# Kernel tuning notes

Measured on AMD Instinct MI355X. Metric: run time of the kernel, lower is better.

## Reference

```python
import jax, jax.numpy as jnp
import numpy as np

B, T, D, H = 2, 2048, 1024, 16
DK = D // H  # 64
LN_EPS = 1e-5


def softmax_one(x, axis=-1):
    # softmax with an extra +1 in the denominator (allows 'attend to nothing')
    x = x - jax.lax.stop_gradient(jnp.max(x, axis=axis, keepdims=True))
    ex = jnp.exp(x)
    return ex / (1.0 + jnp.sum(ex, axis=axis, keepdims=True))


def setup_inputs() -> dict:
    rng = jax.random.key(0)
    ks = jax.random.split(rng, 16)
    s = 0.02  # param init scale
    return {
        "query": jax.random.normal(ks[0], (B, T, D), jnp.float32),
        "key": jax.random.normal(ks[1], (B, T, D), jnp.float32),
        "value": jax.random.normal(ks[2], (B, T, D), jnp.float32),
        "Wq": jax.random.normal(ks[3], (D, D), jnp.float32) * s,
        "bq": jnp.zeros((D,), jnp.float32),
        "Wk": jax.random.normal(ks[4], (D, D), jnp.float32) * s,
        "bk": jnp.zeros((D,), jnp.float32),
        "Wv": jax.random.normal(ks[5], (D, D), jnp.float32) * s,
        "bv": jnp.zeros((D,), jnp.float32),
        "Wo": jax.random.normal(ks[6], (D, D), jnp.float32) * s,
        "bo": jnp.zeros((D,), jnp.float32),
        "gamma": jnp.ones((D,), jnp.float32),
        "beta": jnp.zeros((D,), jnp.float32),
    }


def reference(query, key, value, Wq, bq, Wk, bk, Wv, bv, Wo, bo, gamma, beta):
    # qkv projections; torch Linear: y = x @ W.T + b
    q = (query @ Wq.T + bq).reshape(B, T, H, DK).transpose(0, 2, 1, 3)  # b h t d
    k = (key @ Wk.T + bk).reshape(B, T, H, DK).transpose(0, 2, 1, 3)
    v = (value @ Wv.T + bv).reshape(B, T, H, DK).transpose(0, 2, 1, 3)

    scores = jnp.einsum("bhqd,bhkd->bhqk", q, k) / np.sqrt(DK).astype(np.float32)
    attn = softmax_one(scores, axis=-1)  # mask=None path; dropout = identity (eval)

    x = jnp.einsum("bhqk,bhkd->bhqd", attn, v)  # [B,H,T,DK]
    x = x.transpose(0, 2, 1, 3).reshape(B, T, D)
    out = x @ Wo.T + bo

    # residual + LayerNorm
    y = query + out
    mu = jnp.mean(y, axis=-1, keepdims=True)
    var = jnp.mean(jnp.square(y - mu), axis=-1, keepdims=True)
    y = (y - mu) * jax.lax.rsqrt(var + LN_EPS) * gamma + beta
    return (y, attn)
```

## Files before the change

### kernel.cpp

```cpp
#include <hip/hip_runtime.h>
#include <hip/hip_bf16.h>
#include <math.h>

#define Bb 2
#define Tt 2048
#define Dd 1024
#define Hh 16
#define DKk 64

typedef __bf16 bf16_t;
typedef __bf16 bf16x8 __attribute__((ext_vector_type(8)));
typedef __bf16 bf16x4 __attribute__((ext_vector_type(4)));
typedef float f32x4 __attribute__((ext_vector_type(4)));

__device__ __forceinline__ void async16(const void* gsrc, void* ldst) {
  void* g = const_cast<void*>(gsrc);
  __builtin_amdgcn_global_load_lds(
      (__attribute__((address_space(1))) void*)g,
      (__attribute__((address_space(3))) void*)ldst, 16, 0, 0);
}

__device__ __forceinline__ bf16x8 cvt8(const float4 a, const float4 b) {
  bf16x8 o;
  o[0] = (bf16_t)a.x; o[1] = (bf16_t)a.y; o[2] = (bf16_t)a.z; o[3] = (bf16_t)a.w;
  o[4] = (bf16_t)b.x; o[5] = (bf16_t)b.y; o[6] = (bf16_t)b.z; o[7] = (bf16_t)b.w;
  return o;
}

#define LDSW(p, row, ch) \
  (*(const bf16x8*)((const char*)(p) + (row) * 128 + ((((ch) ^ (row)) & 7) << 4)))

#define BM 128
#define BN 128
#define BK 64

__global__ __launch_bounds__(256) void gemm_f32_bt_bias(
    const float* __restrict__ A, const float* __restrict__ Bw,
    const float* __restrict__ bias, bf16_t* __restrict__ C,
    int M, int N, int K) {
  __shared__ bf16_t As[BM * BK];
  __shared__ bf16_t Bs[BN * BK];
  const int tid = threadIdx.x;
  const int lane = tid & 63;
  const int w = tid >> 6;
  const int wy = w >> 1, wx = w & 1;
  const int m0 = blockIdx.y * BM, n0 = blockIdx.x * BN;
  const int q = lane >> 4, cc = lane & 15;
  const int srow = lane >> 3;
  const int scol = (lane & 7) * 8;

  f32x4 acc[4][4] = {};

  for (int k0 = 0; k0 < K; k0 += BK) {
    __syncthreads();
#pragma unroll
    for (int i = 0; i < 4; ++i) {
      const int row = (w * 4 + i) * 8 + srow;
      const float* ap = A + (size_t)(m0 + row) * K + k0 + scol;
      const float* bp = Bw + (size_t)(n0 + row) * K + k0 + scol;
      *(bf16x8*)(As + row * BK + scol) =
          cvt8(*(const float4*)ap, *(const float4*)(ap + 4));
      *(bf16x8*)(Bs + row * BK + scol) =
          cvt8(*(const float4*)bp, *(const float4*)(bp + 4));
    }
    __syncthreads();
#pragma unroll
    for (int kk = 0; kk < 2; ++kk) {
      bf16x8 af[4], bfr[4];
#pragma unroll
      for (int i = 0; i < 4; ++i)
        af[i] = *(const bf16x8*)(As + (wy * 64 + i * 16 + cc) * BK + kk * 32 + q * 8);
#pragma unroll
      for (int j = 0; j < 4; ++j)
        bfr[j] = *(const bf16x8*)(Bs + (wx * 64 + j * 16 + cc) * BK + kk * 32 + q * 8);
#pragma unroll
      for (int i = 0; i < 4; ++i)
#pragma unroll
        for (int j = 0; j < 4; ++j)
          acc[i][j] = __builtin_amdgcn_mfma_f32_16x16x32_bf16(af[i], bfr[j], acc[i][j], 0, 0, 0);
    }
  }

#pragma unroll
  for (int j = 0; j < 4; ++j) {
    const int col = n0 + wx * 64 + j * 16 + cc;
    const float bv = bias[col];
#pragma unroll
    for (int i = 0; i < 4; ++i) {
      const int row = m0 + wy * 64 + i * 16 + q * 4;
#pragma unroll
      for (int r = 0; r < 4; ++r)
        C[(size_t)(row + r) * N + col] = (bf16_t)(acc[i][j][r] + bv);
    }
  }
}

__global__ __launch_bounds__(256) void gemm_f32_bt_bias_vt(
    const float* __restrict__ A, const float* __restrict__ Bw,
    const float* __restrict__ bias, bf16_t* __restrict__ C,
    int M, int N, int K) {
  __shared__ bf16_t As[BM * BK];
  __shared__ bf16_t Bs[BN * BK];
  const int tid = threadIdx.x;
  const int lane = tid & 63;
  const int w = tid >> 6;
  const int wy = w >> 1, wx = w & 1;
  const int m0 = blockIdx.y * BM, n0 = blockIdx.x * BN;
  const int q = lane >> 4, cc = lane & 15;
  const int srow = lane >> 3;
  const int scol = (lane & 7) * 8;

  f32x4 acc[4][4] = {};

  for (int k0 = 0; k0 < K; k0 += BK) {
    __syncthreads();
#pragma unroll
    for (int i = 0; i < 4; ++i) {
      const int row = (w * 4 + i) * 8 + srow;
      const float* ap = A + (size_t)(m0 + row) * K + k0 + scol;
      const float* bp = Bw + (size_t)(n0 + row) * K + k0 + scol;
      *(bf16x8*)(As + row * BK + scol) =
          cvt8(*(const float4*)ap, *(const float4*)(ap + 4));
      *(bf16x8*)(Bs + row * BK + scol) =
          cvt8(*(const float4*)bp, *(const float4*)(bp + 4));
    }
    __syncthreads();
#pragma unroll
    for (int kk = 0; kk < 2; ++kk) {
      bf16x8 af[4], bfr[4];
#pragma unroll
      for (int i = 0; i < 4; ++i)
        af[i] = *(const bf16x8*)(As + (wy * 64 + i * 16 + cc) * BK + kk * 32 + q * 8);
#pragma unroll
      for (int j = 0; j < 4; ++j)
        bfr[j] = *(const bf16x8*)(Bs + (wx * 64 + j * 16 + cc) * BK + kk * 32 + q * 8);
#pragma unroll
      for (int i = 0; i < 4; ++i)
#pragma unroll
        for (int j = 0; j < 4; ++j)
          acc[i][j] = __builtin_amdgcn_mfma_f32_16x16x32_bf16(af[i], bfr[j], acc[i][j], 0, 0, 0);
    }
  }

  const int bdx = m0 >> 11;
  const int t00 = (m0 & (Tt - 1)) + wy * 64;
#pragma unroll
  for (int j = 0; j < 4; ++j) {
    const int col = n0 + wx * 64 + j * 16 + cc;
    const float bv = bias[col];
    const size_t rowbase = ((size_t)(bdx * Dd + col)) * Tt;
#pragma unroll
    for (int i = 0; i < 4; ++i) {
      const int t0 = t00 + i * 16 + q * 4;
      bf16x4 pk;
#pragma unroll
      for (int r = 0; r < 4; ++r) pk[r] = (bf16_t)(acc[i][j][r] + bv);
      *(bf16x4*)(C + rowbase + t0) = pk;
    }
  }
}

__global__ __launch_bounds__(256) void gemm_bf16a_f32b_bias(
    const bf16_t* __restrict__ A, const float* __restrict__ Bw,
    const float* __restrict__ bias, bf16_t* __restrict__ C,
    int M, int N, int K) {
  __shared__ bf16_t As[BM * BK];
  __shared__ bf16_t Bs[BN * BK];
  const int tid = threadIdx.x;
  const int lane = tid & 63;
  const int w = tid >> 6;
  const int wy = w >> 1, wx = w & 1;
  const int m0 = blockIdx.y * BM, n0 = blockIdx.x * BN;
  const int q = lane >> 4, cc = lane & 15;
  const int srow = lane >> 3;
  const int scol = (lane & 7) * 8;

  f32x4 acc[4][4] = {};

  for (int k0 = 0; k0 < K; k0 += BK) {
    __syncthreads();
#pragma unroll
    for (int i = 0; i < 4; ++i) {
      const int r0 = w * 32 + i * 8;
      async16(A + (size_t)(m0 + r0 + srow) * K + k0 + scol, As + r0 * BK);
    }
#pragma unroll
    for (int i = 0; i < 4; ++i) {
      const int row = (w * 4 + i) * 8 + srow;
      const float* bp = Bw + (size_t)(n0 + row) * K + k0 + scol;
      *(bf16x8*)(Bs + row * BK + scol) =
          cvt8(*(const float4*)bp, *(const float4*)(bp + 4));
    }
    __syncthreads();
#pragma unroll
    for (int kk = 0; kk < 2; ++kk) {
      bf16x8 af[4], bfr[4];
#pragma unroll
      for (int i = 0; i < 4; ++i)
        af[i] = *(const bf16x8*)(As + (wy * 64 + i * 16 + cc) * BK + kk * 32 + q * 8);
#pragma unroll
      for (int j = 0; j < 4; ++j)
        bfr[j] = *(const bf16x8*)(Bs + (wx * 64 + j * 16 + cc) * BK + kk * 32 + q * 8);
#pragma unroll
      for (int i = 0; i < 4; ++i)
#pragma unroll
        for (int j = 0; j < 4; ++j)
          acc[i][j] = __builtin_amdgcn_mfma_f32_16x16x32_bf16(af[i], bfr[j], acc[i][j], 0, 0, 0);
    }
  }

#pragma unroll
  for (int j = 0; j < 4; ++j) {
    const int col = n0 + wx * 64 + j * 16 + cc;
    const float bv = bias[col];
#pragma unroll
    for (int i = 0; i < 4; ++i) {
      const int row = m0 + wy * 64 + i * 16 + q * 4;
#pragma unroll
      for (int r = 0; r < 4; ++r)
        C[(size_t)(row + r) * N + col] = (bf16_t)(acc[i][j][r] + bv);
    }
  }
}

__global__ __launch_bounds__(256) void attn_fused(
    const bf16_t* __restrict__ Qm, const bf16_t* __restrict__ Km,
    const bf16_t* __restrict__ Vt_g,
    float* __restrict__ attn_out,
    bf16_t* __restrict__ Xb) {
  __shared__ bf16_t Qs[64 * 64];
  __shared__ bf16_t Ks[2][64 * 64];
  __shared__ bf16_t Vs[2][64 * 64];
  __shared__ bf16_t Ps[64 * 64];

  const int tid = threadIdx.x;
  const int lane = tid & 63;
  const int w = tid >> 6;
  const int qt = blockIdx.x, h = blockIdx.y, b = blockIdx.z;
  const int q = lane >> 4, cc = lane & 15;
  const size_t base = (size_t)b * Tt * Dd + (size_t)h * DKk;
  const size_t vbase = ((size_t)(b * Hh + h) * DKk) * Tt;
  const int srow = lane >> 3;
  const int gcol = ((lane & 7) ^ srow) * 8;
  const float CL = 0.18033688f;
  const float C2 = 11.54156028f;

#pragma unroll
  for (int i = 0; i < 2; ++i) {
    const int r0 = w * 16 + i * 8;
    async16(Qm + base + (size_t)(qt * 64 + r0 + srow) * Dd + gcol, Qs + r0 * 64);
    async16(Km + base + (size_t)(r0 + srow) * Dd + gcol, Ks[0] + r0 * 64);
  }

  float Mp[4], Lp[4];
#pragma unroll
  for (int r = 0; r < 4; ++r) { Mp[r] = -3.0e38f; Lp[r] = 0.f; }

  for (int kt = 0; kt < 32; ++kt) {
    __syncthreads();
    if (kt < 31) {
      bf16_t* kd = Ks[(kt + 1) & 1];
#pragma unroll
      for (int i = 0; i < 2; ++i) {
        const int r0 = w * 16 + i * 8;
        async16(Km + base + (size_t)((kt + 1) * 64 + r0 + srow) * Dd + gcol, kd + r0 * 64);
      }
    }
    const bf16_t* kc = Ks[kt & 1];
    f32x4 acc[4] = {};
    __builtin_amdgcn_s_setprio(1);
#pragma unroll
    for (int kk = 0; kk < 2; ++kk) {
      const bf16x8 af = LDSW(Qs, w * 16 + cc, kk * 4 + q);
#pragma unroll
      for (int j = 0; j < 4; ++j) {
        const bf16x8 bfr = LDSW(kc, j * 16 + cc, kk * 4 + q);
        acc[j] = __builtin_amdgcn_mfma_f32_16x16x32_bf16(af, bfr, acc[j], 0, 0, 0);
      }
    }
    __builtin_amdgcn_s_setprio(0);
#pragma unroll
    for (int r = 0; r < 4; ++r) {
      Mp[r] = fmaxf(Mp[r], fmaxf(fmaxf(acc[0][r], acc[1][r]),
                                 fmaxf(acc[2][r], acc[3][r])));
      Lp[r] += exp2f(fmaf(acc[0][r], CL, -C2)) + exp2f(fmaf(acc[1][r], CL, -C2)) +
               exp2f(fmaf(acc[2][r], CL, -C2)) + exp2f(fmaf(acc[3][r], CL, -C2));
    }
  }

  float inv1[4];
#pragma unroll
  for (int r = 0; r < 4; ++r) {
    float mx = Mp[r];
#pragma unroll
    for (int msk = 1; msk < 16; msk <<= 1) mx = fmaxf(mx, __shfl_xor(mx, msk));
    float ls = Lp[r];
#pragma unroll
    for (int msk = 1; msk < 16; msk <<= 1) ls += __shfl_xor(ls, msk);
    inv1[r] = 1.0f / (exp2f(fmaf(mx, CL, -C2)) + ls);
  }

#pragma unroll
  for (int i = 0; i < 2; ++i) {
    const int r0 = w * 16 + i * 8;
    async16(Km + base + (size_t)(r0 + srow) * Dd + gcol, Ks[0] + r0 * 64);
    async16(Vt_g + vbase + (size_t)(r0 + srow) * Tt + gcol, Vs[0] + r0 * 64);
  }

  f32x4 xacc[4] = {};
  const size_t arowbase = ((size_t)(b * Hh + h) * Tt + (size_t)qt * 64) * Tt;

  for (int kt = 0; kt < 32; ++kt) {
    __syncthreads();
    if (kt < 31) {
      bf16_t* kd = Ks[(kt + 1) & 1];
      bf16_t* vd = Vs[(kt + 1) & 1];
#pragma unroll
      for (int i = 0; i < 2; ++i) {
        const int r0 = w * 16 + i * 8;
        async16(Km + base + (size_t)((kt + 1) * 64 + r0 + srow) * Dd + gcol, kd + r0 * 64);
        async16(Vt_g + vbase + (size_t)(r0 + srow) * Tt + (kt + 1) * 64 + gcol, vd + r0 * 64);
      }
    }
    const bf16_t* kc = Ks[kt & 1];
    const bf16_t* vc = Vs[kt & 1];

    f32x4 acc[4] = {};
    __builtin_amdgcn_s_setprio(1);
#pragma unroll
    for (int kk = 0; kk < 2; ++kk) {
      const bf16x8 af = LDSW(Qs, w * 16 + cc, kk * 4 + q);
#pragma unroll
      for (int j = 0; j < 4; ++j) {
        const bf16x8 bfr = LDSW(kc, j * 16 + cc, kk * 4 + q);
        acc[j] = __builtin_amdgcn_mfma_f32_16x16x32_bf16(af, bfr, acc[j], 0, 0, 0);
      }
    }
    __builtin_amdgcn_s_setprio(0);

#pragma unroll
    for (int j = 0; j < 4; ++j) {
      const int pcol = j * 16 + cc;
#pragma unroll
      for (int r = 0; r < 4; ++r) {
        const int prow = w * 16 + q * 4 + r;
        const float p = exp2f(fmaf(acc[j][r], CL, -C2)) * inv1[r];
        attn_out[arowbase + (size_t)prow * Tt + kt * 64 + pcol] = p;
        *(bf16_t*)((char*)Ps + prow * 128 + ((pcol * 2) ^ ((prow & 7) << 4))) = (bf16_t)p;
      }
    }

    __builtin_amdgcn_s_setprio(1);
#pragma unroll
    for (int kk = 0; kk < 2; ++kk) {
      const bf16x8 af = LDSW(Ps, w * 16 + cc, kk * 4 + q);
#pragma unroll
      for (int j = 0; j < 4; ++j) {
        const bf16x8 bfr = LDSW(vc, j * 16 + cc, kk * 4 + q);
        xacc[j] = __builtin_amdgcn_mfma_f32_16x16x32_bf16(af, bfr, xacc[j], 0, 0, 0);
      }
    }
    __builtin_amdgcn_s_setprio(0);
  }

#pragma unroll
  for (int j = 0; j < 4; ++j)
#pragma unroll
    for (int r = 0; r < 4; ++r) {
      const int row = qt * 64 + w * 16 + q * 4 + r;
      Xb[base + (size_t)row * Dd + j * 16 + cc] = (bf16_t)xacc[j][r];
    }
}

__global__ __launch_bounds__(256) void ln_kernel(
    const float* __restrict__ resid, const bf16_t* __restrict__ O,
    const float* __restrict__ gamma, const float* __restrict__ beta,
    float* __restrict__ out) {
  const int row = blockIdx.x;
  const int tid = threadIdx.x;
  const size_t roff = (size_t)row * Dd + tid * 4;
  const float4 rv = *(const float4*)(resid + roff);
  const bf16x4 ov = *(const bf16x4*)(O + roff);
  const float y0 = rv.x + (float)ov.x;
  const float y1 = rv.y + (float)ov.y;
  const float y2 = rv.z + (float)ov.z;
  const float y3 = rv.w + (float)ov.w;
  float s = y0 + y1 + y2 + y3;
  float s2 = y0 * y0 + y1 * y1 + y2 * y2 + y3 * y3;
#pragma unroll
  for (int msk = 1; msk < 64; msk <<= 1) {
    s += __shfl_xor(s, msk);
    s2 += __shfl_xor(s2, msk);
  }
  __shared__ float red[8];
  const int w = tid >> 6;
  if ((tid & 63) == 0) { red[w] = s; red[4 + w] = s2; }
  __syncthreads();
  s = red[0] + red[1] + red[2] + red[3];
  s2 = red[4] + red[5] + red[6] + red[7];
  const float mu = s * (1.f / Dd);
  const float rstd = rsqrtf(s2 * (1.f / Dd) - mu * mu + 1e-5f);
  const float4 gv = *(const float4*)(gamma + tid * 4);
  const float4 bv = *(const float4*)(beta + tid * 4);
  float4 o;
  o.x = (y0 - mu) * rstd * gv.x + bv.x;
  o.y = (y1 - mu) * rstd * gv.y + bv.y;
  o.z = (y2 - mu) * rstd * gv.z + bv.z;
  o.w = (y3 - mu) * rstd * gv.w + bv.w;
  *(float4*)(out + roff) = o;
}

extern "C" void kernel_launch(void* const* d_in, const int* in_sizes, int n_in,
                              void* d_out, int out_size, void* d_ws, size_t ws_size,
                              hipStream_t stream) {
  const float* query = (const float*)d_in[0];
  const float* key = (const float*)d_in[1];
  const float* value = (const float*)d_in[2];
  const float* Wq = (const float*)d_in[3];
  const float* bq = (const float*)d_in[4];
  const float* Wk = (const float*)d_in[5];
  const float* bk = (const float*)d_in[6];
  const float* Wv = (const float*)d_in[7];
  const float* bv = (const float*)d_in[8];
  const float* Wo = (const float*)d_in[9];
  const float* bo = (const float*)d_in[10];
  const float* gamma = (const float*)d_in[11];
  const float* beta = (const float*)d_in[12];

  float* y_out = (float*)d_out;
  float* attn_out = y_out + (size_t)Bb * Tt * Dd;

  char* p = (char*)d_ws;
  const size_t nTD = (size_t)Bb * Tt * Dd;
  bf16_t* Qb = (bf16_t*)p;  p += nTD * 2;
  bf16_t* Kb = (bf16_t*)p;  p += nTD * 2;
  bf16_t* VtG = (bf16_t*)p; p += nTD * 2;
  bf16_t* Xb = (bf16_t*)p;  p += nTD * 2;
  bf16_t* Ob = (bf16_t*)p;  p += nTD * 2;

  dim3 gg(Dd / BN, (Bb * Tt) / BM);
  gemm_f32_bt_bias<<<gg, 256, 0, stream>>>(query, Wq, bq, Qb, Bb * Tt, Dd, Dd);
  gemm_f32_bt_bias<<<gg, 256, 0, stream>>>(key, Wk, bk, Kb, Bb * Tt, Dd, Dd);
  gemm_f32_bt_bias_vt<<<gg, 256, 0, stream>>>(value, Wv, bv, VtG, Bb * Tt, Dd, Dd);

  dim3 ga(Tt / 64, Hh, Bb);
  attn_fused<<<ga, 256, 0, stream>>>(Qb, Kb, VtG, attn_out, Xb);

  gemm_bf16a_f32b_bias<<<gg, 256, 0, stream>>>(Xb, Wo, bo, Ob, Bb * Tt, Dd, Dd);

  ln_kernel<<<Bb * Tt, 256, 0, stream>>>(query, Ob, gamma, beta, y_out);
}
```

Measured before the change: 921.9 us.

## Merge QKV GEMMs into one launch, shrink tiles, stage attn probs in LDS

The three projection GEMMs become a single launch over a z-dimension, and both GEMM kernels shrink the M tile from 128 to 64 so more blocks run per launch. In attention, the fp32 probabilities are staged in each wave's slice of the just-consumed K buffer, then written to the attn output as coalesced 16-byte stores instead of scattered scalar stores. The bf16 A operand for the PV MFMA is read back from that same staging, which removes the separate P buffer. The cost is an extra barrier per key tile and more LDS round-trips, and the smaller GEMM tiles give less data reuse per block.

```diff
diff --git a/kernel.cpp b/kernel.cpp
--- a/kernel.cpp
+++ b/kernel.cpp
@@ -30,195 +30,164 @@
 #define LDSW(p, row, ch) \
   (*(const bf16x8*)((const char*)(p) + (row) * 128 + ((((ch) ^ (row)) & 7) << 4)))
 
-#define BM 128
-#define BN 128
-#define BK 64
-
-__global__ __launch_bounds__(256) void gemm_f32_bt_bias(
-    const float* __restrict__ A, const float* __restrict__ Bw,
-    const float* __restrict__ bias, bf16_t* __restrict__ C,
-    int M, int N, int K) {
-  __shared__ bf16_t As[BM * BK];
-  __shared__ bf16_t Bs[BN * BK];
+#define GM 4096
+#define GN 1024
+#define GK 1024
+#define BM2 64
+#define BN2 128
+#define BK2 64
+
+__global__ __launch_bounds__(256) void gemm_qkv(
+    const float* __restrict__ Aq, const float* __restrict__ Ak,
+    const float* __restrict__ Av, const float* __restrict__ Wqp,
+    const float* __restrict__ Wkp, const float* __restrict__ Wvp,
+    const float* __restrict__ bqp, const float* __restrict__ bkp,
+    const float* __restrict__ bvp, bf16_t* __restrict__ Cq,
+    bf16_t* __restrict__ Ck, bf16_t* __restrict__ Cv) {
+  __shared__ bf16_t As[BM2 * BK2];
+  __shared__ bf16_t Bs[BN2 * BK2];
+  const int z = blockIdx.z;
+  const float* A = (z == 0) ? Aq : (z == 1) ? Ak : Av;
+  const float* Bw = (z == 0) ? Wqp : (z == 1) ? Wkp : Wvp;
+  const float* bias = (z == 0) ? bqp : (z == 1) ? bkp : bvp;
+
   const int tid = threadIdx.x;
   const int lane = tid & 63;
   const int w = tid >> 6;
   const int wy = w >> 1, wx = w & 1;
-  const int m0 = blockIdx.y * BM, n0 = blockIdx.x * BN;
+  const int m0 = blockIdx.y * BM2, n0 = blockIdx.x * BN2;
   const int q = lane >> 4, cc = lane & 15;
   const int srow = lane >> 3;
   const int scol = (lane & 7) * 8;
 
-  f32x4 acc[4][4] = {};
-
-  for (int k0 = 0; k0 < K; k0 += BK) {
-    __syncthreads();
+  f32x4 acc[2][4] = {};
+
+  for (int k0 = 0; k0 < GK; k0 += BK2) {
+    __syncthreads();
+#pragma unroll
+    for (int i = 0; i < 2; ++i) {
+      const int row = w * 16 + i * 8 + srow;
+      const float* ap = A + (size_t)(m0 + row) * GK + k0 + scol;
+      *(bf16x8*)(As + row * BK2 + scol) =
+          cvt8(*(const float4*)ap, *(const float4*)(ap + 4));
+    }
 #pragma unroll
     for (int i = 0; i < 4; ++i) {
       const int row = (w * 4 + i) * 8 + srow;
-      const float* ap = A + (size_t)(m0 + row) * K + k0 + scol;
-      const float* bp = Bw + (size_t)(n0 + row) * K + k0 + scol;
-      *(bf16x8*)(As + row * BK + scol) =
-          cvt8(*(const float4*)ap, *(const float4*)(ap + 4));
-      *(bf16x8*)(Bs + row * BK + scol) =
+      const float* bp = Bw + (size_t)(n0 + row) * GK + k0 + scol;
+      *(bf16x8*)(Bs + row * BK2 + scol) =
           cvt8(*(const float4*)bp, *(const float4*)(bp + 4));
     }
     __syncthreads();
 #pragma unroll
     for (int kk = 0; kk < 2; ++kk) {
-      bf16x8 af[4], bfr[4];
-#pragma unroll
-      for (int i = 0; i < 4; ++i)
-        af[i] = *(const bf16x8*)(As + (wy * 64 + i * 16 + cc) * BK + kk * 32 + q * 8);
+      bf16x8 af[2], bfr[4];
+#pragma unroll
+      for (int i = 0; i < 2; ++i)
+        af[i] = *(const bf16x8*)(As + (wy * 32 + i * 16 + cc) * BK2 + kk * 32 + q * 8);
 #pragma unroll
       for (int j = 0; j < 4; ++j)
-        bfr[j] = *(const bf16x8*)(Bs + (wx * 64 + j * 16 + cc) * BK + kk * 32 + q * 8);
-#pragma unroll
-      for (int i = 0; i < 4; ++i)
+        bfr[j] = *(const bf16x8*)(Bs + (wx * 64 + j * 16 + cc) * BK2 + kk * 32 + q * 8);
+#pragma unroll
+      for (int i = 0; i < 2; ++i)
 #pragma unroll
         for (int j = 0; j < 4; ++j)
           acc[i][j] = __builtin_amdgcn_mfma_f32_16x16x32_bf16(af[i], bfr[j], acc[i][j], 0, 0, 0);
     }
   }
 
-#pragma unroll
-  for (int j = 0; j < 4; ++j) {
-    const int col = n0 + wx * 64 + j * 16 + cc;
-    const float bv = bias[col];
-#pragma unroll
-    for (int i = 0; i < 4; ++i) {
-      const int row = m0 + wy * 64 + i * 16 + q * 4;
-#pragma unroll
-      for (int r = 0; r < 4; ++r)
-        C[(size_t)(row + r) * N + col] = (bf16_t)(acc[i][j][r] + bv);
-    }
-  }
-}
-
-__global__ __launch_bounds__(256) void gemm_f32_bt_bias_vt(
-    const float* __restrict__ A, const float* __restrict__ Bw,
-    const float* __restrict__ bias, bf16_t* __restrict__ C,
-    int M, int N, int K) {
-  __shared__ bf16_t As[BM * BK];
-  __shared__ bf16_t Bs[BN * BK];
+  if (z < 2) {
+    bf16_t* C = z ? Ck : Cq;
+#pragma unroll
+    for (int j = 0; j < 4; ++j) {
+      const int col = n0 + wx * 64 + j * 16 + cc;
+      const float bv = bias[col];
+#pragma unroll
+      for (int i = 0; i < 2; ++i) {
+        const int row = m0 + wy * 32 + i * 16 + q * 4;
+#pragma unroll
+        for (int r = 0; r < 4; ++r)
+          C[(size_t)(row + r) * GN + col] = (bf16_t)(acc[i][j][r] + bv);
+      }
+    }
+  } else {
+    const int bdx = m0 >> 11;
+    const int t00 = (m0 & (Tt - 1)) + wy * 32;
+#pragma unroll
+    for (int j = 0; j < 4; ++j) {
+      const int col = n0 + wx * 64 + j * 16 + cc;
+      const float bv = bias[col];
+      const size_t rowbase = ((size_t)(bdx * Dd + col)) * Tt;
+#pragma unroll
+      for (int i = 0; i < 2; ++i) {
+        const int t0 = t00 + i * 16 + q * 4;
+        bf16x4 pk;
+#pragma unroll
+        for (int r = 0; r < 4; ++r) pk[r] = (bf16_t)(acc[i][j][r] + bv);
+        *(bf16x4*)(Cv + rowbase + t0) = pk;
+      }
+    }
+  }
+}
+
+__global__ __launch_bounds__(256) void gemm_obf16(
+    const bf16_t* __restrict__ A, const float* __restrict__ Bw,
+    const float* __restrict__ bias, bf16_t* __restrict__ C) {
+  __shared__ bf16_t As[BM2 * BK2];
+  __shared__ bf16_t Bs[BN2 * BK2];
   const int tid = threadIdx.x;
   const int lane = tid & 63;
   const int w = tid >> 6;
   const int wy = w >> 1, wx = w & 1;
-  const int m0 = blockIdx.y * BM, n0 = blockIdx.x * BN;
+  const int m0 = blockIdx.y * BM2, n0 = blockIdx.x * BN2;
   const int q = lane >> 4, cc = lane & 15;
   const int srow = lane >> 3;
   const int scol = (lane & 7) * 8;
 
-  f32x4 acc[4][4] = {};
-
-  for (int k0 = 0; k0 < K; k0 += BK) {
-    __syncthreads();
+  f32x4 acc[2][4] = {};
+
+  for (int k0 = 0; k0 < GK; k0 += BK2) {
+    __syncthreads();
+#pragma unroll
+    for (int i = 0; i < 2; ++i) {
+      const int r0 = w * 16 + i * 8;
+      async16(A + (size_t)(m0 + r0 + srow) * GK + k0 + scol, As + r0 * BK2);
+    }
 #pragma unroll
     for (int i = 0; i < 4; ++i) {
       const int row = (w * 4 + i) * 8 + srow;
-      const float* ap = A + (size_t)(m0 + row) * K + k0 + scol;
-      const float* bp = Bw + (size_t)(n0 + row) * K + k0 + scol;
-      *(bf16x8*)(As + row * BK + scol) =
-          cvt8(*(const float4*)ap, *(const float4*)(ap + 4));
-      *(bf16x8*)(Bs + row * BK + scol) =
+      const float* bp = Bw + (size_t)(n0 + row) * GK + k0 + scol;
+      *(bf16x8*)(Bs + row * BK2 + scol) =
           cvt8(*(const float4*)bp, *(const float4*)(bp + 4));
     }
     __syncthreads();
 #pragma unroll
     for (int kk = 0; kk < 2; ++kk) {
-      bf16x8 af[4], bfr[4];
-#pragma unroll
-      for (int i = 0; i < 4; ++i)
-        af[i] = *(const bf16x8*)(As + (wy * 64 + i * 16 + cc) * BK + kk * 32 + q * 8);
+      bf16x8 af[2], bfr[4];
+#pragma unroll
+      for (int i = 0; i < 2; ++i)
+        af[i] = *(const bf16x8*)(As + (wy * 32 + i * 16 + cc) * BK2 + kk * 32 + q * 8);
 #pragma unroll
       for (int j = 0; j < 4; ++j)
-        bfr[j] = *(const bf16x8*)(Bs + (wx * 64 + j * 16 + cc) * BK + kk * 32 + q * 8);
-#pragma unroll
-      for (int i = 0; i < 4; ++i)
+        bfr[j] = *(const bf16x8*)(Bs + (wx * 64 + j * 16 + cc) * BK2 + kk * 32 + q * 8);
+#pragma unroll
+      for (int i = 0; i < 2; ++i)
 #pragma unroll
         for (int j = 0; j < 4; ++j)
           acc[i][j] = __builtin_amdgcn_mfma_f32_16x16x32_bf16(af[i], bfr[j], acc[i][j], 0, 0, 0);
     }
   }
 
-  const int bdx = m0 >> 11;
-  const int t00 = (m0 & (Tt - 1)) + wy * 64;
 #pragma unroll
   for (int j = 0; j < 4; ++j) {
     const int col = n0 + wx * 64 + j * 16 + cc;
     const float bv = bias[col];
-    const size_t rowbase = ((size_t)(bdx * Dd + col)) * Tt;
-#pragma unroll
-    for (int i = 0; i < 4; ++i) {
-      const int t0 = t00 + i * 16 + q * 4;
-      bf16x4 pk;
-#pragma unroll
-      for (int r = 0; r < 4; ++r) pk[r] = (bf16_t)(acc[i][j][r] + bv);
-      *(bf16x4*)(C + rowbase + t0) = pk;
-    }
-  }
-}
-
-__global__ __launch_bounds__(256) void gemm_bf16a_f32b_bias(
-    const bf16_t* __restrict__ A, const float* __restrict__ Bw,
-    const float* __restrict__ bias, bf16_t* __restrict__ C,
-    int M, int N, int K) {
-  __shared__ bf16_t As[BM * BK];
-  __shared__ bf16_t Bs[BN * BK];
-  const int tid = threadIdx.x;
-  const int lane = tid & 63;
-  const int w = tid >> 6;
-  const int wy = w >> 1, wx = w & 1;
-  const int m0 = blockIdx.y * BM, n0 = blockIdx.x * BN;
-  const int q = lane >> 4, cc = lane & 15;
-  const int srow = lane >> 3;
-  const int scol = (lane & 7) * 8;
-
-  f32x4 acc[4][4] = {};
-
-  for (int k0 = 0; k0 < K; k0 += BK) {
-    __syncthreads();
-#pragma unroll
-    for (int i = 0; i < 4; ++i) {
-      const int r0 = w * 32 + i * 8;
-      async16(A + (size_t)(m0 + r0 + srow) * K + k0 + scol, As + r0 * BK);
-    }
-#pragma unroll
-    for (int i = 0; i < 4; ++i) {
-      const int row = (w * 4 + i) * 8 + srow;
-      const float* bp = Bw + (size_t)(n0 + row) * K + k0 + scol;
-      *(bf16x8*)(Bs + row * BK + scol) =
-          cvt8(*(const float4*)bp, *(const float4*)(bp + 4));
-    }
-    __syncthreads();
-#pragma unroll
-    for (int kk = 0; kk < 2; ++kk) {
-      bf16x8 af[4], bfr[4];
-#pragma unroll
-      for (int i = 0; i < 4; ++i)
-        af[i] = *(const bf16x8*)(As + (wy * 64 + i * 16 + cc) * BK + kk * 32 + q * 8);
-#pragma unroll
-      for (int j = 0; j < 4; ++j)
-        bfr[j] = *(const bf16x8*)(Bs + (wx * 64 + j * 16 + cc) * BK + kk * 32 + q * 8);
-#pragma unroll
-      for (int i = 0; i < 4; ++i)
-#pragma unroll
-        for (int j = 0; j < 4; ++j)
-          acc[i][j] = __builtin_amdgcn_mfma_f32_16x16x32_bf16(af[i], bfr[j], acc[i][j], 0, 0, 0);
-    }
-  }
-
-#pragma unroll
-  for (int j = 0; j < 4; ++j) {
-    const int col = n0 + wx * 64 + j * 16 + cc;
-    const float bv = bias[col];
-#pragma unroll
-    for (int i = 0; i < 4; ++i) {
-      const int row = m0 + wy * 64 + i * 16 + q * 4;
+#pragma unroll
+    for (int i = 0; i < 2; ++i) {
+      const int row = m0 + wy * 32 + i * 16 + q * 4;
 #pragma unroll
       for (int r = 0; r < 4; ++r)
-        C[(size_t)(row + r) * N + col] = (bf16_t)(acc[i][j][r] + bv);
+        C[(size_t)(row + r) * GN + col] = (bf16_t)(acc[i][j][r] + bv);
     }
   }
 }
@@ -231,7 +200,6 @@
   __shared__ bf16_t Qs[64 * 64];
   __shared__ bf16_t Ks[2][64 * 64];
   __shared__ bf16_t Vs[2][64 * 64];
-  __shared__ bf16_t Ps[64 * 64];
 
   const int tid = threadIdx.x;
   const int lane = tid & 63;
@@ -242,6 +210,8 @@
   const size_t vbase = ((size_t)(b * Hh + h) * DKk) * Tt;
   const int srow = lane >> 3;
   const int gcol = ((lane & 7) ^ srow) * 8;
+  const int l2 = lane >> 2;
+  const int lc = lane & 3;
   const float CL = 0.18033688f;
   const float C2 = 11.54156028f;
 
@@ -338,29 +308,48 @@
     }
     __builtin_amdgcn_s_setprio(0);
 
-#pragma unroll
-    for (int j = 0; j < 4; ++j) {
-      const int pcol = j * 16 + cc;
-#pragma unroll
-      for (int r = 0; r < 4; ++r) {
-        const int prow = w * 16 + q * 4 + r;
-        const float p = exp2f(fmaf(acc[j][r], CL, -C2)) * inv1[r];
-        attn_out[arowbase + (size_t)prow * Tt + kt * 64 + pcol] = p;
-        *(bf16_t*)((char*)Ps + prow * 128 + ((pcol * 2) ^ ((prow & 7) << 4))) = (bf16_t)p;
-      }
-    }
-
-    __builtin_amdgcn_s_setprio(1);
-#pragma unroll
-    for (int kk = 0; kk < 2; ++kk) {
-      const bf16x8 af = LDSW(Ps, w * 16 + cc, kk * 4 + q);
+    __builtin_amdgcn_sched_barrier(0);
+    __builtin_amdgcn_s_barrier();
+
+    char* sfw = (char*)(&Ks[kt & 1][0]) + w * 2048;
+#pragma unroll
+    for (int half = 0; half < 2; ++half) {
+#pragma unroll
+      for (int jj = 0; jj < 2; ++jj) {
+        const int j = half * 2 + jj;
+#pragma unroll
+        for (int r = 0; r < 4; ++r) {
+          const int row16 = q * 4 + r;
+          const float p = exp2f(fmaf(acc[j][r], CL, -C2)) * inv1[r];
+          *(float*)(sfw + row16 * 128 +
+                    (((jj * 16 + cc) * 4) ^ ((row16 & 7) << 4))) = p;
+        }
+      }
+#pragma unroll
+      for (int s = 0; s < 2; ++s) {
+        const int ch = lc + 4 * s;
+        const f32x4 v = *(const f32x4*)(sfw + l2 * 128 +
+                                        ((ch * 16) ^ ((l2 & 7) << 4)));
+        const int prow = w * 16 + l2;
+        *(f32x4*)(attn_out + arowbase + (size_t)prow * Tt + kt * 64 +
+                  half * 32 + ch * 4) = v;
+      }
+      const char* p0 = sfw + cc * 128;
+      const f32x4 a = *(const f32x4*)(p0 + ((q * 32) ^ ((cc & 7) << 4)));
+      const f32x4 bb = *(const f32x4*)(p0 + ((q * 32 + 16) ^ ((cc & 7) << 4)));
+      bf16x8 af;
+      af[0] = (bf16_t)a[0]; af[1] = (bf16_t)a[1];
+      af[2] = (bf16_t)a[2]; af[3] = (bf16_t)a[3];
+      af[4] = (bf16_t)bb[0]; af[5] = (bf16_t)bb[1];
+      af[6] = (bf16_t)bb[2]; af[7] = (bf16_t)bb[3];
+      __builtin_amdgcn_s_setprio(1);
 #pragma unroll
       for (int j = 0; j < 4; ++j) {
-        const bf16x8 bfr = LDSW(vc, j * 16 + cc, kk * 4 + q);
+        const bf16x8 bfr = LDSW(vc, j * 16 + cc, half * 4 + q);
         xacc[j] = __builtin_amdgcn_mfma_f32_16x16x32_bf16(af, bfr, xacc[j], 0, 0, 0);
       }
-    }
-    __builtin_amdgcn_s_setprio(0);
+      __builtin_amdgcn_s_setprio(0);
+    }
   }
 
 #pragma unroll
@@ -438,15 +427,15 @@
   bf16_t* Xb = (bf16_t*)p;  p += nTD * 2;
   bf16_t* Ob = (bf16_t*)p;  p += nTD * 2;
 
-  dim3 gg(Dd / BN, (Bb * Tt) / BM);
-  gemm_f32_bt_bias<<<gg, 256, 0, stream>>>(query, Wq, bq, Qb, Bb * Tt, Dd, Dd);
-  gemm_f32_bt_bias<<<gg, 256, 0, stream>>>(key, Wk, bk, Kb, Bb * Tt, Dd, Dd);
-  gemm_f32_bt_bias_vt<<<gg, 256, 0, stream>>>(value, Wv, bv, VtG, Bb * Tt, Dd, Dd);
+  dim3 gqkv(GN / BN2, GM / BM2, 3);
+  gemm_qkv<<<gqkv, 256, 0, stream>>>(query, key, value, Wq, Wk, Wv,
+                                     bq, bk, bv, Qb, Kb, VtG);
 
   dim3 ga(Tt / 64, Hh, Bb);
   attn_fused<<<ga, 256, 0, stream>>>(Qb, Kb, VtG, attn_out, Xb);
 
-  gemm_bf16a_f32b_bias<<<gg, 256, 0, stream>>>(Xb, Wo, bo, Ob, Bb * Tt, Dd, Dd);
+  dim3 go(GN / BN2, GM / BM2);
+  gemm_obf16<<<go, 256, 0, stream>>>(Xb, Wo, bo, Ob);
 
   ln_kernel<<<Bb * Tt, 256, 0, stream>>>(query, Ob, gamma, beta, y_out);
 }
```

New measurement: 911.7 us. About the same (-1.1%).
